# Kernel optimization log

Measured on AMD Instinct MI355X. Metric: run time of the kernel, lower is better.

## Reference

```python
import jax, jax.numpy as jnp
import numpy as np

L, B, T, N, M = 2, 32, 256, 1024, 1024  # layers, batch, time, input feat, hidden


def setup_inputs() -> dict:
    key = jax.random.key(0)
    ks = jax.random.split(key, 7)
    s = 0.02  # weight init scale
    return {
        "x": jax.random.normal(ks[0], (B, T, N), dtype=jnp.float32),
        "h": jax.random.normal(ks[1], (L, B, M), dtype=jnp.float32) * 0.1,
        "c": jax.random.normal(ks[2], (L, B, M), dtype=jnp.float32) * 0.1,
        "Wih": jax.random.normal(ks[3], (L, 4 * M, N), dtype=jnp.float32) * s,
        "Whh": jax.random.normal(ks[4], (L, 4 * M, M), dtype=jnp.float32) * s,
        "bih": jnp.zeros((L, 4 * M), dtype=jnp.float32),
        "bhh": jnp.zeros((L, 4 * M), dtype=jnp.float32),
    }


def _lstm_cell(x_t, h_t, c_t, Wih_l, Whh_l, b_l):
    # gates: [i | f | g | o], matching torch.nn.LSTMCell layout
    gates = x_t @ Wih_l.T + h_t @ Whh_l.T + b_l  # (B, 4M)
    i, f, g, o = jnp.split(gates, 4, axis=-1)
    i, f, o = jax.nn.sigmoid(i), jax.nn.sigmoid(f), jax.nn.sigmoid(o)
    c_new = f * c_t + i * jnp.tanh(g)
    h_new = o * jnp.tanh(c_new)
    return h_new, c_new


def reference(x, h, c, Wih, Whh, bih, bhh):
    b_sum = bih + bhh  # (L, 4M)

    def step(carry, x_t):
        h_cur, c_cur = carry  # each (L, B, M)
        hs, cs = [], []
        inp = x_t
        for l in range(L):  # small fixed layer loop
            h_l, c_l = _lstm_cell(inp, h_cur[l], c_cur[l], Wih[l], Whh[l], b_sum[l])
            hs.append(h_l)
            cs.append(c_l)
            inp = h_l
        return (jnp.stack(hs, 0), jnp.stack(cs, 0)), inp  # emit top-layer h

    (h_final, c_final), outs_tbm = jax.lax.scan(step, (h, c), jnp.swapaxes(x, 0, 1))
    outs = jnp.swapaxes(outs_tbm, 0, 1)  # (B, T, M)
    return outs, h_final, c_final
```

## Files before the change

### kernel.cpp

```cpp
#include <hip/hip_runtime.h>


typedef __bf16 bf16x8 __attribute__((ext_vector_type(8)));
typedef float  f32x4  __attribute__((ext_vector_type(4)));
typedef unsigned u32x4 __attribute__((ext_vector_type(4)));

__device__ __forceinline__ unsigned short f2bf(float f) {
    union { float f; unsigned u; } v; v.f = f;
    unsigned u = v.u;
    unsigned r = u + 0x7fffu + ((u >> 16) & 1u);
    return (unsigned short)(r >> 16);
}
__device__ __forceinline__ float sigmoidf_fast(float x) {
    return 1.0f / (1.0f + __expf(-x));
}
__device__ __forceinline__ float tanhf_fast(float x) {
    return 1.0f - 2.0f / (__expf(2.0f * x) + 1.0f);
}

__global__ void cvt_w_concat(const float* __restrict__ src,
                             unsigned short* __restrict__ dst, int off, int n4) {
    int i = blockIdx.x * blockDim.x + threadIdx.x;
    int stride = gridDim.x * blockDim.x;
    for (; i < n4; i += stride) {
        float4 v = ((const float4*)src)[i];
        ushort4 o;
        o.x = f2bf(v.x); o.y = f2bf(v.y); o.z = f2bf(v.z); o.w = f2bf(v.w);
        int row = i >> 8;
        int c4  = i & 255;
        *(ushort4*)&dst[(size_t)row * 2048 + off + c4 * 4] = o;
    }
}

__global__ void cvt_x_tiles(const float* __restrict__ x,
                            unsigned short* __restrict__ xT) {
    int t = blockIdx.x, tid = threadIdx.x;
    unsigned short* tile = xT + (size_t)t * 32768;
    for (int b = 0; b < 32; ++b) {
        float4 v = *(const float4*)&x[((size_t)b * 256 + t) * 1024 + tid * 4];
        ushort4 o;
        o.x = f2bf(v.x); o.y = f2bf(v.y); o.z = f2bf(v.z); o.w = f2bf(v.w);
        *(ushort4*)&tile[(tid >> 2) * 512 + b * 16 + (tid & 3) * 4] = o;
    }
}

__global__ void cvt_h0_tiles(const float* __restrict__ h0,
                             unsigned short* __restrict__ h0T) {
    int l = blockIdx.x, tid = threadIdx.x;
    unsigned short* tile = h0T + (size_t)l * 32768;
    for (int b = 0; b < 32; ++b) {
        float4 v = *(const float4*)&h0[((size_t)l * 32 + b) * 1024 + tid * 4];
        ushort4 o;
        o.x = f2bf(v.x); o.y = f2bf(v.y); o.z = f2bf(v.z); o.w = f2bf(v.w);
        *(ushort4*)&tile[(tid >> 2) * 512 + b * 16 + (tid & 3) * 4] = o;
    }
}

__global__ void out_transpose(const float* __restrict__ outT,
                              float* __restrict__ out) {
    int t = blockIdx.x, tid = threadIdx.x;
    const float* tile = outT + (size_t)t * 32768;
    for (int b = 0; b < 32; ++b) {
        float4 v = *(const float4*)&tile[(tid >> 2) * 512 + b * 16 + (tid & 3) * 4];
        *(float4*)&out[((size_t)b * 256 + t) * 1024 + tid * 4] = v;
    }
}

__device__ __forceinline__ void pollge(const unsigned* fp, unsigned tgt) {
    while (true) {
        unsigned v = __hip_atomic_load(fp, __ATOMIC_RELAXED,
                                       __HIP_MEMORY_SCOPE_AGENT);
        if (__all((int)(v >= tgt))) break;
        __builtin_amdgcn_s_sleep(1);
    }
}

__global__ __launch_bounds__(256, 1) void lstm_fused(
    const unsigned short* __restrict__ Wcat,
    const unsigned short* __restrict__ xT,
    unsigned short* __restrict__ seqT,
    const unsigned short* __restrict__ h0T,
    unsigned short* __restrict__ hparT,
    float* __restrict__ outT,
    const float* __restrict__ c0,
    const float* __restrict__ bih, const float* __restrict__ bhh,
    float* __restrict__ out, unsigned int* flags)
{
    __shared__ __align__(16) unsigned short bufH[32][1024];
    __shared__ __align__(16) unsigned short bufX[32][1024];

    const int tid  = threadIdx.x;
    const int lane = tid & 63;
    const int w    = tid >> 6;
    const int l    = blockIdx.x >> 6;
    const int bidl = blockIdx.x & 63;
    const int m0   = bidl * 16;
    const int n    = lane & 15;
    const int g    = lane >> 4;
    const int lk   = g * 8;
    const int nn7  = n & 7;

    char* const bH = (char*)&bufH[0][0];
    char* const bX = (char*)&bufX[0][0];
    float (*gred)[2][4][16][20] = (float (*)[2][4][16][20])bX;

    bf16x8 wx[32], wh[32];
    const unsigned short* Wl = Wcat + (size_t)l * 4096 * 2048;
    #pragma unroll
    for (int ct = 0; ct < 4; ct++) {
        int vc = ct * 16 + n;
        size_t jrow = (size_t)((vc & 3) * 1024 + m0 + (vc >> 2));
        #pragma unroll
        for (int kc = 0; kc < 8; kc++) {
            wx[ct*8+kc] = *(const bf16x8*)&Wl[jrow*2048 +        w*256 + kc*32 + lk];
            wh[ct*8+kc] = *(const bf16x8*)&Wl[jrow*2048 + 1024 + w*256 + kc*32 + lk];
        }
    }

    const int eb = lane >> 1;
    const int q  = lane & 1;
    const int em = m0 + 4 * w + 2 * q;
    float bs0[4], bs1[4];
    #pragma unroll
    for (int gg = 0; gg < 4; gg++) {
        bs0[gg] = bih[l*4096 + gg*1024 + em]     + bhh[l*4096 + gg*1024 + em];
        bs1[gg] = bih[l*4096 + gg*1024 + em + 1] + bhh[l*4096 + gg*1024 + em + 1];
    }
    float2 creg = *(const float2*)&c0[(size_t)l * 32768 + eb * 1024 + em];
    float2 hlast = {0.f, 0.f};
    const int uh = eb >> 4, urow = eb & 15;

    const int exOff = bidl * 1024 + eb * 32 + (4 * w + 2 * q) * 2;
    const int outOff = bidl * 2048 + eb * 64 + (4 * w + 2 * q) * 4;

    const int sb     = lane >> 1;
    const int halfk  = lane & 1;
    const int srcOff = w * 16384 + sb * 32 + halfk * 16;
    const int sbRow  = sb * 2048;
    const int ldsCol = w * 512 + halfk * 16;
    const int swz    = (sb & 7) << 4;

    const int hb64 = (nn7 >> 2) * 64;
    const int gx16 = (g ^ (nn7 & 3)) * 16;
    const int rOffA0 = n * 2048 + w * 512 + gx16 + hb64;
    const int rOffA1 = n * 2048 + w * 512 + gx16 + (64 - hb64);

    f32x4 acc0[4] = {}, acc1[4] = {};
    u32x4 hv[16];

    auto issue = [&](const char* tb, bool byp) {
        const char* gp = tb + srcOff;
        if (byp) {
            #pragma unroll
            for (int si = 0; si < 16; si++)
                asm volatile("global_load_dwordx4 %0, %1, off sc0 sc1"
                             : "=v"(hv[si]) : "v"(gp + si * 1024) : "memory");
        } else {
            #pragma unroll
            for (int si = 0; si < 16; si++)
                asm volatile("global_load_dwordx4 %0, %1, off"
                             : "=v"(hv[si]) : "v"(gp + si * 1024) : "memory");
        }
    };

    auto stage_gemm_h = [&](const char* tb) {
        const char* gp = tb + srcOff;
        #pragma unroll
        for (int si = 0; si < 16; si++)
            asm volatile("global_load_dwordx4 %0, %1, off sc0 sc1"
                         : "=v"(hv[si]) : "v"(gp + si * 1024) : "memory");
        const char* pA0 = bH + rOffA0;
        const char* pA1 = bH + rOffA1;
        const char* pB0 = pA0 + 16 * 2048;
        const char* pB1 = pA1 + 16 * 2048;
#define SGRP(G4, VM) \
        asm volatile("s_waitcnt vmcnt(" VM ")" ::: "memory"); \
        _Pragma("unroll") \
        for (int si = 4*(G4); si < 4*(G4)+4; si++) \
            *(u32x4*)(bH + sbRow + ((ldsCol + si*32) ^ swz)) = hv[si]; \
        { \
            bf16x8 a0 = *(const bf16x8*)(pA0 + (G4)*128); \
            bf16x8 a1 = *(const bf16x8*)(pB0 + (G4)*128); \
            _Pragma("unroll") \
            for (int ct = 0; ct < 4; ct++) { \
                acc0[ct] = __builtin_amdgcn_mfma_f32_16x16x32_bf16(a0, wh[ct*8+2*(G4)],   acc0[ct],0,0,0); \
                acc1[ct] = __builtin_amdgcn_mfma_f32_16x16x32_bf16(a1, wh[ct*8+2*(G4)],   acc1[ct],0,0,0); \
            } \
            bf16x8 b0 = *(const bf16x8*)(pA1 + (G4)*128); \
            bf16x8 b1 = *(const bf16x8*)(pB1 + (G4)*128); \
            _Pragma("unroll") \
            for (int ct = 0; ct < 4; ct++) { \
                acc0[ct] = __builtin_amdgcn_mfma_f32_16x16x32_bf16(b0, wh[ct*8+2*(G4)+1], acc0[ct],0,0,0); \
                acc1[ct] = __builtin_amdgcn_mfma_f32_16x16x32_bf16(b1, wh[ct*8+2*(G4)+1], acc1[ct],0,0,0); \
            } \
        }
        SGRP(0, "12") SGRP(1, "8") SGRP(2, "4") SGRP(3, "0")
#undef SGRP
    };

    if (l == 0) {
        issue((const char*)xT, false);
        asm volatile("s_waitcnt vmcnt(0)" ::: "memory");
        #pragma unroll
        for (int si = 0; si < 16; si++)
            *(u32x4*)(bX + sbRow + ((ldsCol + si * 32) ^ swz)) = hv[si];
        const char* pA0 = bX + rOffA0;
        const char* pA1 = bX + rOffA1;
        const char* pB0 = pA0 + 16 * 2048;
        const char* pB1 = pA1 + 16 * 2048;
        #pragma unroll
        for (int kc2 = 0; kc2 < 4; kc2++) {
            bf16x8 a0 = *(const bf16x8*)(pA0 + kc2 * 128);
            bf16x8 a1 = *(const bf16x8*)(pB0 + kc2 * 128);
            #pragma unroll
            for (int ct = 0; ct < 4; ct++) {
                acc0[ct] = __builtin_amdgcn_mfma_f32_16x16x32_bf16(a0, wx[ct*8+2*kc2],   acc0[ct],0,0,0);
                acc1[ct] = __builtin_amdgcn_mfma_f32_16x16x32_bf16(a1, wx[ct*8+2*kc2],   acc1[ct],0,0,0);
            }
            bf16x8 b0 = *(const bf16x8*)(pA1 + kc2 * 128);
            bf16x8 b1 = *(const bf16x8*)(pB1 + kc2 * 128);
            #pragma unroll
            for (int ct = 0; ct < 4; ct++) {
                acc0[ct] = __builtin_amdgcn_mfma_f32_16x16x32_bf16(b0, wx[ct*8+2*kc2+1], acc0[ct],0,0,0);
                acc1[ct] = __builtin_amdgcn_mfma_f32_16x16x32_bf16(b1, wx[ct*8+2*kc2+1], acc1[ct],0,0,0);
            }
        }
    }
    __syncthreads();

    const int lag = l * 2;
    #pragma unroll 1
    for (int s = 0; s < 258; s++) {
        const int  t    = s - lag;
        const bool act  = (t >= 0) && (t < 256);
        const int  tn   = t + 1;
        const bool xact = (tn >= ((l == 0) ? 1 : 0)) && (tn <= 255);
        const char* xsrc = (l == 0) ? (const char*)(xT   + (size_t)tn * 32768)
                                    : (const char*)(seqT + (size_t)tn * 32768);

        if (act) {
            const char* hb = (t == 0)
                ? (const char*)(h0T + (size_t)l * 32768)
                : (l == 0 ? (const char*)(seqT + (size_t)(t - 1) * 32768)
                          : (const char*)(hparT + (size_t)((t - 1) & 1) * 32768));
            stage_gemm_h(hb);

            if (xact) issue(xsrc, l == 1);

            {
                int r0 = g * 4;
                #pragma unroll
                for (int ct = 0; ct < 4; ct++) {
                    *(f32x4*)&gred[w][0][ct][n][r0] = acc0[ct];
                    *(f32x4*)&gred[w][1][ct][n][r0] = acc1[ct];
                }
            }
            __syncthreads();
            float g8[8];
            #pragma unroll
            for (int j = 0; j < 8; j++) {
                g8[j] = (gred[0][uh][w][8*q+j][urow] + gred[1][uh][w][8*q+j][urow])
                      + (gred[2][uh][w][8*q+j][urow] + gred[3][uh][w][8*q+j][urow]);
            }
            float gi0 = g8[0] + bs0[0], gf0 = g8[1] + bs0[1];
            float gg0 = g8[2] + bs0[2], go0 = g8[3] + bs0[3];
            float gi1 = g8[4] + bs1[0], gf1 = g8[5] + bs1[1];
            float gg1 = g8[6] + bs1[2], go1 = g8[7] + bs1[3];

            float c0n = sigmoidf_fast(gf0) * creg.x + sigmoidf_fast(gi0) * tanhf_fast(gg0);
            float c1n = sigmoidf_fast(gf1) * creg.y + sigmoidf_fast(gi1) * tanhf_fast(gg1);
            float h0v = sigmoidf_fast(go0) * tanhf_fast(c0n);
            float h1v = sigmoidf_fast(go1) * tanhf_fast(c1n);
            creg.x = c0n; creg.y = c1n;
            hlast.x = h0v; hlast.y = h1v;

            unsigned hp = (unsigned)f2bf(h0v) | ((unsigned)f2bf(h1v) << 16);
            {
                char* dp = (l == 0)
                    ? (char*)(seqT  + (size_t)t * 32768)       + exOff
                    : (char*)(hparT + (size_t)(t & 1) * 32768) + exOff;
                asm volatile("global_store_dword %0, %1, off sc0 sc1"
                             :: "v"(dp), "v"(hp) : "memory");
                if (l == 1) {
                    float2 hv2 = {h0v, h1v};
                    *(float2*)((char*)outT + (size_t)t * 131072 + outOff) = hv2;
                }
                asm volatile("s_waitcnt vmcnt(0)" ::: "memory");
            }
            __syncthreads();
            if (tid == 0)
                __hip_atomic_store(flags + l * 64 + bidl, (unsigned)(s + 1),
                                   __ATOMIC_RELAXED, __HIP_MEMORY_SCOPE_AGENT);
        } else {
            if (tid == 0)
                __hip_atomic_store(flags + l * 64 + bidl, (unsigned)(s + 1),
                                   __ATOMIC_RELAXED, __HIP_MEMORY_SCOPE_AGENT);
            if (xact) issue(xsrc, l == 1);
        }

        if (xact) {
            #pragma unroll
            for (int ct = 0; ct < 4; ct++) {
                acc0[ct] = (f32x4){0.f, 0.f, 0.f, 0.f};
                acc1[ct] = (f32x4){0.f, 0.f, 0.f, 0.f};
            }
            const char* pA0 = bX + rOffA0;
            const char* pA1 = bX + rOffA1;
            const char* pB0 = pA0 + 16 * 2048;
            const char* pB1 = pA1 + 16 * 2048;
#define TGRP(G4, VM) \
            asm volatile("s_waitcnt vmcnt(" VM ")" ::: "memory"); \
            _Pragma("unroll") \
            for (int si = 4*(G4); si < 4*(G4)+4; si++) \
                *(u32x4*)(bX + sbRow + ((ldsCol + si*32) ^ swz)) = hv[si]; \
            { \
                bf16x8 a0 = *(const bf16x8*)(pA0 + (G4)*128); \
                bf16x8 a1 = *(const bf16x8*)(pB0 + (G4)*128); \
                _Pragma("unroll") \
                for (int ct = 0; ct < 4; ct++) { \
                    acc0[ct] = __builtin_amdgcn_mfma_f32_16x16x32_bf16(a0, wx[ct*8+2*(G4)],   acc0[ct],0,0,0); \
                    acc1[ct] = __builtin_amdgcn_mfma_f32_16x16x32_bf16(a1, wx[ct*8+2*(G4)],   acc1[ct],0,0,0); \
                } \
                bf16x8 b0 = *(const bf16x8*)(pA1 + (G4)*128); \
                bf16x8 b1 = *(const bf16x8*)(pB1 + (G4)*128); \
                _Pragma("unroll") \
                for (int ct = 0; ct < 4; ct++) { \
                    acc0[ct] = __builtin_amdgcn_mfma_f32_16x16x32_bf16(b0, wx[ct*8+2*(G4)+1], acc0[ct],0,0,0); \
                    acc1[ct] = __builtin_amdgcn_mfma_f32_16x16x32_bf16(b1, wx[ct*8+2*(G4)+1], acc1[ct],0,0,0); \
                } \
            }
            TGRP(0, "12") TGRP(1, "8") TGRP(2, "4") TGRP(3, "0")
#undef TGRP
        }

        if (tid < 128) pollge(flags + tid, (unsigned)(s + 1));
        __syncthreads();
    }

    float* hF = out + (size_t)8192 * 1024 + (size_t)l * 32768;
    float* cF = out + (size_t)8192 * 1024 + 65536 + (size_t)l * 32768;
    float2 hf2 = {hlast.x, hlast.y};
    *(float2*)&hF[eb * 1024 + em] = hf2;
    float2 cf2 = {creg.x, creg.y};
    *(float2*)&cF[eb * 1024 + em] = cf2;
}

extern "C" void kernel_launch(void* const* d_in, const int* in_sizes, int n_in,
                              void* d_out, int out_size, void* d_ws, size_t ws_size,
                              hipStream_t stream)
{
    const float* x   = (const float*)d_in[0];
    const float* h0  = (const float*)d_in[1];
    const float* c0  = (const float*)d_in[2];
    const float* Wih = (const float*)d_in[3];
    const float* Whh = (const float*)d_in[4];
    const float* bih = (const float*)d_in[5];
    const float* bhh = (const float*)d_in[6];
    float* out = (float*)d_out;

    char* p = (char*)d_ws;
    unsigned short* xT    = (unsigned short*)p; p += (size_t)256 * 32768 * 2;
    unsigned short* seqT  = (unsigned short*)p; p += (size_t)256 * 32768 * 2;
    unsigned short* Wcat  = (unsigned short*)p; p += (size_t)2 * 4096 * 2048 * 2;
    unsigned short* h0T   = (unsigned short*)p; p += (size_t)2 * 32768 * 2;
    unsigned short* hparT = (unsigned short*)p; p += (size_t)2 * 32768 * 2;
    float*          outT  = (float*)p;          p += (size_t)256 * 32768 * 4;
    unsigned int*   flags = (unsigned int*)p;   p += 4096;

    hipMemsetAsync(flags, 0, 4096, stream);
    cvt_w_concat<<<1024, 256, 0, stream>>>(Wih, Wcat, 0,    2 * 4096 * 256);
    cvt_w_concat<<<1024, 256, 0, stream>>>(Whh, Wcat, 1024, 2 * 4096 * 256);
    cvt_x_tiles<<<256, 256, 0, stream>>>(x, xT);
    cvt_h0_tiles<<<2, 256, 0, stream>>>(h0, h0T);

    lstm_fused<<<128, 256, 0, stream>>>(Wcat, xT, seqT, h0T, hparT, outT,
                                        c0, bih, bhh, out, flags);

    out_transpose<<<256, 256, 0, stream>>>(outT, out);
}
```

Measured before the change: 1.335 ms.

## Move x-projection GEMM into critical step, overlap with h loads, swizzle gate reduction

Before, the off-critical-path section only stages the next x tile into LDS. The x-projection MFMAs now run at the start of each active step, while the h tile's global loads are in flight, instead of after the barrier and flag write. The cross-wave gate reduction buffer moves from the padded float array in bufX into bufH with an XOR swizzle, likely to avoid bank conflicts and keep bufX free for the staged x. This puts the x GEMM on the recurrent critical path, which can lengthen each step if the h loads return before it finishes.

```diff
diff --git a/kernel.cpp b/kernel.cpp
--- a/kernel.cpp
+++ b/kernel.cpp
@@ -102,7 +102,6 @@
 
     char* const bH = (char*)&bufH[0][0];
     char* const bX = (char*)&bufX[0][0];
-    float (*gred)[2][4][16][20] = (float (*)[2][4][16][20])bX;
 
     bf16x8 wx[32], wh[32];
     const unsigned short* Wl = Wcat + (size_t)l * 4096 * 2048;
@@ -130,7 +129,7 @@
     float2 hlast = {0.f, 0.f};
     const int uh = eb >> 4, urow = eb & 15;
 
-    const int exOff = bidl * 1024 + eb * 32 + (4 * w + 2 * q) * 2;
+    const int exOff  = bidl * 1024 + eb * 32 + (4 * w + 2 * q) * 2;
     const int outOff = bidl * 2048 + eb * 64 + (4 * w + 2 * q) * 4;
 
     const int sb     = lane >> 1;
@@ -145,7 +144,9 @@
     const int rOffA0 = n * 2048 + w * 512 + gx16 + hb64;
     const int rOffA1 = n * 2048 + w * 512 + gx16 + (64 - hb64);
 
-    f32x4 acc0[4] = {}, acc1[4] = {};
+    const int nsw = (n & 7) << 4;
+
+    f32x4 acc0[4], acc1[4];
     u32x4 hv[16];
 
     auto issue = [&](const char* tb, bool byp) {
@@ -163,47 +164,7 @@
         }
     };
 
-    auto stage_gemm_h = [&](const char* tb) {
-        const char* gp = tb + srcOff;
-        #pragma unroll
-        for (int si = 0; si < 16; si++)
-            asm volatile("global_load_dwordx4 %0, %1, off sc0 sc1"
-                         : "=v"(hv[si]) : "v"(gp + si * 1024) : "memory");
-        const char* pA0 = bH + rOffA0;
-        const char* pA1 = bH + rOffA1;
-        const char* pB0 = pA0 + 16 * 2048;
-        const char* pB1 = pA1 + 16 * 2048;
-#define SGRP(G4, VM) \
-        asm volatile("s_waitcnt vmcnt(" VM ")" ::: "memory"); \
-        _Pragma("unroll") \
-        for (int si = 4*(G4); si < 4*(G4)+4; si++) \
-            *(u32x4*)(bH + sbRow + ((ldsCol + si*32) ^ swz)) = hv[si]; \
-        { \
-            bf16x8 a0 = *(const bf16x8*)(pA0 + (G4)*128); \
-            bf16x8 a1 = *(const bf16x8*)(pB0 + (G4)*128); \
-            _Pragma("unroll") \
-            for (int ct = 0; ct < 4; ct++) { \
-                acc0[ct] = __builtin_amdgcn_mfma_f32_16x16x32_bf16(a0, wh[ct*8+2*(G4)],   acc0[ct],0,0,0); \
-                acc1[ct] = __builtin_amdgcn_mfma_f32_16x16x32_bf16(a1, wh[ct*8+2*(G4)],   acc1[ct],0,0,0); \
-            } \
-            bf16x8 b0 = *(const bf16x8*)(pA1 + (G4)*128); \
-            bf16x8 b1 = *(const bf16x8*)(pB1 + (G4)*128); \
-            _Pragma("unroll") \
-            for (int ct = 0; ct < 4; ct++) { \
-                acc0[ct] = __builtin_amdgcn_mfma_f32_16x16x32_bf16(b0, wh[ct*8+2*(G4)+1], acc0[ct],0,0,0); \
-                acc1[ct] = __builtin_amdgcn_mfma_f32_16x16x32_bf16(b1, wh[ct*8+2*(G4)+1], acc1[ct],0,0,0); \
-            } \
-        }
-        SGRP(0, "12") SGRP(1, "8") SGRP(2, "4") SGRP(3, "0")
-#undef SGRP
-    };
-
-    if (l == 0) {
-        issue((const char*)xT, false);
-        asm volatile("s_waitcnt vmcnt(0)" ::: "memory");
-        #pragma unroll
-        for (int si = 0; si < 16; si++)
-            *(u32x4*)(bX + sbRow + ((ldsCol + si * 32) ^ swz)) = hv[si];
+    auto xgemm = [&]() {
         const char* pA0 = bX + rOffA0;
         const char* pA1 = bX + rOffA1;
         const char* pB0 = pA0 + 16 * 2048;
@@ -225,6 +186,14 @@
                 acc1[ct] = __builtin_amdgcn_mfma_f32_16x16x32_bf16(b1, wx[ct*8+2*kc2+1], acc1[ct],0,0,0);
             }
         }
+    };
+
+    if (l == 0) {
+        issue((const char*)xT, false);
+        asm volatile("s_waitcnt vmcnt(0)" ::: "memory");
+        #pragma unroll
+        for (int si = 0; si < 16; si++)
+            *(u32x4*)(bX + sbRow + ((ldsCol + si * 32) ^ swz)) = hv[si];
     }
     __syncthreads();
 
@@ -243,24 +212,72 @@
                 ? (const char*)(h0T + (size_t)l * 32768)
                 : (l == 0 ? (const char*)(seqT + (size_t)(t - 1) * 32768)
                           : (const char*)(hparT + (size_t)((t - 1) & 1) * 32768));
-            stage_gemm_h(hb);
+            {
+                const char* gp = hb + srcOff;
+                #pragma unroll
+                for (int si = 0; si < 16; si++)
+                    asm volatile("global_load_dwordx4 %0, %1, off sc0 sc1"
+                                 : "=v"(hv[si]) : "v"(gp + si * 1024) : "memory");
+            }
+
+            #pragma unroll
+            for (int ct = 0; ct < 4; ct++) {
+                acc0[ct] = (f32x4){0.f, 0.f, 0.f, 0.f};
+                acc1[ct] = (f32x4){0.f, 0.f, 0.f, 0.f};
+            }
+            xgemm();
+
+            {
+                const char* pA0 = bH + rOffA0;
+                const char* pA1 = bH + rOffA1;
+                const char* pB0 = pA0 + 16 * 2048;
+                const char* pB1 = pA1 + 16 * 2048;
+#define SGRP(G4, VM) \
+                asm volatile("s_waitcnt vmcnt(" VM ")" ::: "memory"); \
+                _Pragma("unroll") \
+                for (int si = 4*(G4); si < 4*(G4)+4; si++) \
+                    *(u32x4*)(bH + sbRow + ((ldsCol + si*32) ^ swz)) = hv[si]; \
+                { \
+                    bf16x8 a0 = *(const bf16x8*)(pA0 + (G4)*128); \
+                    bf16x8 a1 = *(const bf16x8*)(pB0 + (G4)*128); \
+                    _Pragma("unroll") \
+                    for (int ct = 0; ct < 4; ct++) { \
+                        acc0[ct] = __builtin_amdgcn_mfma_f32_16x16x32_bf16(a0, wh[ct*8+2*(G4)],   acc0[ct],0,0,0); \
+                        acc1[ct] = __builtin_amdgcn_mfma_f32_16x16x32_bf16(a1, wh[ct*8+2*(G4)],   acc1[ct],0,0,0); \
+                    } \
+                    bf16x8 b0 = *(const bf16x8*)(pA1 + (G4)*128); \
+                    bf16x8 b1 = *(const bf16x8*)(pB1 + (G4)*128); \
+                    _Pragma("unroll") \
+                    for (int ct = 0; ct < 4; ct++) { \
+                        acc0[ct] = __builtin_amdgcn_mfma_f32_16x16x32_bf16(b0, wh[ct*8+2*(G4)+1], acc0[ct],0,0,0); \
+                        acc1[ct] = __builtin_amdgcn_mfma_f32_16x16x32_bf16(b1, wh[ct*8+2*(G4)+1], acc1[ct],0,0,0); \
+                    } \
+                }
+                SGRP(0, "12") SGRP(1, "8") SGRP(2, "4") SGRP(3, "0")
+#undef SGRP
+            }
 
             if (xact) issue(xsrc, l == 1);
 
-            {
-                int r0 = g * 4;
-                #pragma unroll
-                for (int ct = 0; ct < 4; ct++) {
-                    *(f32x4*)&gred[w][0][ct][n][r0] = acc0[ct];
-                    *(f32x4*)&gred[w][1][ct][n][r0] = acc1[ct];
-                }
+            #pragma unroll
+            for (int ct = 0; ct < 4; ct++) {
+                int wb0 = ((0 * 4 + ct) * 16 + n) * 64 + g * 16;
+                int wb1 = ((1 * 4 + ct) * 16 + n) * 64 + g * 16;
+                *(f32x4*)(bH + ((wb0 >> 9) << 11) + w * 512 + ((wb0 & 511) ^ nsw)) = acc0[ct];
+                *(f32x4*)(bH + ((wb1 >> 9) << 11) + w * 512 + ((wb1 & 511) ^ nsw)) = acc1[ct];
             }
             __syncthreads();
             float g8[8];
             #pragma unroll
             for (int j = 0; j < 8; j++) {
-                g8[j] = (gred[0][uh][w][8*q+j][urow] + gred[1][uh][w][8*q+j][urow])
-                      + (gred[2][uh][w][8*q+j][urow] + gred[3][uh][w][8*q+j][urow]);
+                int nn  = 8 * q + j;
+                int wbr = ((uh * 4 + w) * 16 + nn) * 64 + urow * 4;
+                int rowb = (wbr >> 9) << 11;
+                int colb = (wbr & 511) ^ ((nn & 7) << 4);
+                g8[j] = (*(const float*)(bH + rowb + 0 * 512 + colb)
+                       + *(const float*)(bH + rowb + 1 * 512 + colb))
+                      + (*(const float*)(bH + rowb + 2 * 512 + colb)
+                       + *(const float*)(bH + rowb + 3 * 512 + colb));
             }
             float gi0 = g8[0] + bs0[0], gf0 = g8[1] + bs0[1];
             float gg0 = g8[2] + bs0[2], go0 = g8[3] + bs0[3];
@@ -299,38 +316,10 @@
         }
 
         if (xact) {
-            #pragma unroll
-            for (int ct = 0; ct < 4; ct++) {
-                acc0[ct] = (f32x4){0.f, 0.f, 0.f, 0.f};
-                acc1[ct] = (f32x4){0.f, 0.f, 0.f, 0.f};
-            }
-            const char* pA0 = bX + rOffA0;
-            const char* pA1 = bX + rOffA1;
-            const char* pB0 = pA0 + 16 * 2048;
-            const char* pB1 = pA1 + 16 * 2048;
-#define TGRP(G4, VM) \
-            asm volatile("s_waitcnt vmcnt(" VM ")" ::: "memory"); \
-            _Pragma("unroll") \
-            for (int si = 4*(G4); si < 4*(G4)+4; si++) \
-                *(u32x4*)(bX + sbRow + ((ldsCol + si*32) ^ swz)) = hv[si]; \
-            { \
-                bf16x8 a0 = *(const bf16x8*)(pA0 + (G4)*128); \
-                bf16x8 a1 = *(const bf16x8*)(pB0 + (G4)*128); \
-                _Pragma("unroll") \
-                for (int ct = 0; ct < 4; ct++) { \
-                    acc0[ct] = __builtin_amdgcn_mfma_f32_16x16x32_bf16(a0, wx[ct*8+2*(G4)],   acc0[ct],0,0,0); \
-                    acc1[ct] = __builtin_amdgcn_mfma_f32_16x16x32_bf16(a1, wx[ct*8+2*(G4)],   acc1[ct],0,0,0); \
-                } \
-                bf16x8 b0 = *(const bf16x8*)(pA1 + (G4)*128); \
-                bf16x8 b1 = *(const bf16x8*)(pB1 + (G4)*128); \
-                _Pragma("unroll") \
-                for (int ct = 0; ct < 4; ct++) { \
-                    acc0[ct] = __builtin_amdgcn_mfma_f32_16x16x32_bf16(b0, wx[ct*8+2*(G4)+1], acc0[ct],0,0,0); \
-                    acc1[ct] = __builtin_amdgcn_mfma_f32_16x16x32_bf16(b1, wx[ct*8+2*(G4)+1], acc1[ct],0,0,0); \
-                } \
-            }
-            TGRP(0, "12") TGRP(1, "8") TGRP(2, "4") TGRP(3, "0")
-#undef TGRP
+            asm volatile("s_waitcnt vmcnt(0)" ::: "memory");
+            #pragma unroll
+            for (int si = 0; si < 16; si++)
+                *(u32x4*)(bX + sbRow + ((ldsCol + si * 32) ^ swz)) = hv[si];
         }
 
         if (tid < 128) pollge(flags + tid, (unsigned)(s + 1));
```

New measurement: 1.656 ms. +24.1%, slower.
